# Kernel optimization log

Measured on AMD Instinct MI355X. Metric: run time of the kernel, lower is better.

The kernel has to match this reference:

```python
import jax, jax.numpy as jnp
import numpy as np

N_LAYERS = 200
KSIZE = 7
L_IN = 1388
FC_IN = 188   # 1388 - 200*6
FC_OUT = 91


def setup_inputs() -> dict:
    key = jax.random.key(0)
    k_x, k_w, k_b, k_fw, k_fb = jax.random.split(key, 5)
    B = 1024
    x = jax.random.normal(k_x, (B, L_IN), dtype=jnp.float32)
    # Conv1d(1,1,7) weights: torch default init U(-s, s) with s = 1/sqrt(in_ch*k) = 1/sqrt(7)
    s = 1.0 / np.sqrt(KSIZE)
    conv_w = jax.random.uniform(k_w, (N_LAYERS, KSIZE), dtype=jnp.float32, minval=-s, maxval=s)
    conv_b = jax.random.uniform(k_b, (N_LAYERS,), dtype=jnp.float32, minval=-s, maxval=s)
    sf = 1.0 / np.sqrt(FC_IN)
    fc_w = jax.random.uniform(k_fw, (FC_OUT, FC_IN), dtype=jnp.float32, minval=-sf, maxval=sf)
    fc_b = jax.random.uniform(k_fb, (FC_OUT,), dtype=jnp.float32, minval=-sf, maxval=sf)
    return {"x": x, "conv_w": conv_w, "conv_b": conv_b, "fc_w": fc_w, "fc_b": fc_b}


def _conv1(h, w, b):
    # h: [B, L]; cross-correlation with taps w[0..6], valid padding -> [B, L-6]
    L_out = h.shape[1] - (KSIZE - 1)
    acc = w[0] * h[:, 0:L_out]
    for k in range(1, KSIZE):
        acc = acc + w[k] * h[:, k:k + L_out]
    return acc + b


def reference(x, conv_w, conv_b, fc_w, fc_b):
    h = x  # unsqueeze(1) is implicit: single channel handled as [B, L]
    for i in range(N_LAYERS):
        h = _conv1(h, conv_w[i], conv_b[i])
        if i < N_LAYERS - 1:  # last ReLU was popped in the torch module
            h = jax.nn.relu(h)
    # Linear(188, 91) applied to the length dim, then Sigmoid; squeeze channel dim
    out = jax.nn.sigmoid(h @ fc_w.T + fc_b)  # [B, 91]
    return out
```

## Files before the change

kernel.cpp:

```cpp
#include <hip/hip_runtime.h>
#include <math.h>

#define N_LAYERS 200
#define KSIZE 7
#define L_IN 1388
#define FC_IN 188
#define FC_OUT 91
#define NT 256
#define NW 4
#define NSTAGES 13
#define NGROUPS 50
#define LBUF_N 1352

constexpr int lin_(int s)  { return L_IN - 96 * s; }
constexpr int lout_(int s) { return (s < 12) ? L_IN - 96 * (s + 1) : FC_IN; }
constexpr int nlay_(int s) { return (s < 12) ? 16 : 8; }
constexpr int s_R(int s) {
    const int span = lout_(s) / 4 + 1 + 6 * nlay_(s);
    return (span + 63) / 64;
}

__device__ __forceinline__ float dpp_next(float v) {
    return __int_as_float(
        __builtin_amdgcn_mov_dpp(__float_as_int(v), 0x130, 0xf, 0xf, true));
}

struct __align__(16) WG { float w[32]; };

__device__ __forceinline__ void load_wg(WG& wg, const float4* kb4, int g) {
#pragma unroll
    for (int q = 0; q < 8; ++q)
        *reinterpret_cast<float4*>(&wg.w[4 * q]) = kb4[g * 8 + q];
}

template<int R, bool NR3>
__device__ __forceinline__ void run4(float (&r)[7], const WG& wg) {
#pragma unroll
    for (int jj = 0; jj < 4; ++jj) {
        float h[6];
        {
            constexpr int H1 = (R < 6) ? R : 6;
#pragma unroll
            for (int t = 0; t < H1; ++t) h[t] = dpp_next(r[t]);
#pragma unroll
            for (int t = H1; t < 6; ++t) h[t] = dpp_next(h[t - R]);
        }
        const bool relu = !(NR3 && jj == 3);
#pragma unroll
        for (int j = 0; j < R; ++j) {
            float acc = wg.w[28 + jj];
#pragma unroll
            for (int d = 0; d < KSIZE; ++d) {
                const int m = j + d;
                const float src = (m < R) ? r[m] : h[m - R];
                acc = fmaf(wg.w[jj * 7 + d], src, acc);
            }
            r[j] = relu ? fmaxf(acc, 0.0f) : acc;
        }
    }
}

template<int R, bool FINAL>
__device__ __forceinline__ void run_stage_g(float (&r)[7], WG& A,
        const float4* kb4, int g0, int g1) {
#pragma unroll 1
    for (int g = g0; g < g1; g += 2) {
        WG B;
        load_wg(B, kb4, (g + 1 < NGROUPS) ? g + 1 : NGROUPS - 1);
        run4<R, false>(r, A);
        load_wg(A, kb4, (g + 2 < NGROUPS) ? g + 2 : NGROUPS - 1);
        run4<R, FINAL>(r, B);
    }
}

template<int Ro, int Rn>
__device__ __forceinline__ void repack(float (&r)[7], float* lbuf,
                                       int lane, int co, int co1, int cn) {
#pragma unroll
    for (int j = 0; j < Ro; ++j) {
        const int p = co + lane * Ro + j;
        if (p < co1) lbuf[p] = r[j];
    }
    __syncthreads();
#pragma unroll
    for (int j = 0; j < Rn; ++j) r[j] = lbuf[cn + lane * Rn + j];
    __syncthreads();
}

template<int S>
struct Chain {
    __device__ static __forceinline__ void run(float (&r)[7], WG& A,
        const float4* kb4, float* lbuf, int lane, int wid)
    {
        run_stage_g<s_R(S), false>(r, A, kb4, 4 * S, 4 * S + 4);
        const int co  = (wid * lout_(S)) >> 2;
        const int co1 = ((wid + 1) * lout_(S)) >> 2;
        const int cn  = (wid * lout_(S + 1)) >> 2;
        repack<s_R(S), s_R(S + 1)>(r, lbuf, lane, co, co1, cn);
        Chain<S + 1>::run(r, A, kb4, lbuf, lane, wid);
    }
};

template<>
struct Chain<NSTAGES - 1> {
    __device__ static __forceinline__ void run(float (&r)[7], WG& A,
        const float4* kb4, float* lbuf, int lane, int wid)
    {
        constexpr int R = s_R(NSTAGES - 1);
        run_stage_g<R, true>(r, A, kb4, 48, 50);
        const int co  = (wid * FC_IN) >> 2;
        const int co1 = ((wid + 1) * FC_IN) >> 2;
#pragma unroll
        for (int j = 0; j < R; ++j) {
            const int p = co + lane * R + j;
            if (p < co1) lbuf[p] = r[j];
        }
        __syncthreads();
    }
};

__global__ __launch_bounds__(NT, 4) void conv_chain_kernel(
    const float* __restrict__ x,
    const float* __restrict__ conv_w,
    const float* __restrict__ conv_b,
    const float* __restrict__ fc_w,
    const float* __restrict__ fc_b,
    float* __restrict__ out)
{
    __shared__ __align__(16) float lbuf[LBUF_N];
    __shared__ __align__(16) float kbuf[NGROUPS * 32];

    const int row  = blockIdx.x;
    const int tid  = threadIdx.x;
    const int lane = tid & 63;
    const int wid  = tid >> 6;

    for (int i = tid; i < NGROUPS * 32; i += NT) {
        const int g = i >> 5, t = i & 31;
        kbuf[i] = (t < 28) ? conv_w[g * 28 + t] : conv_b[g * 4 + (t - 28)];
    }
    for (int i = tid; i < LBUF_N; i += NT) lbuf[i] = 0.0f;

    float r[7];
    const float* xr = x + (size_t)row * L_IN;
    const int c0 = (wid * lout_(0)) >> 2;
#pragma unroll
    for (int j = 0; j < 7; ++j) {
        const int p = c0 + lane * 7 + j;
        r[j] = (p < L_IN) ? xr[p] : 0.0f;
    }
    __syncthreads();

    WG A;
    const float4* kb4 = reinterpret_cast<const float4*>(kbuf);
    load_wg(A, kb4, 0);

    Chain<0>::run(r, A, kb4, lbuf, lane, wid);

    if (tid < FC_OUT) {
        float acc = fc_b[tid];
        const float4* wp = (const float4*)(fc_w + tid * FC_IN);
        const float4* hp = (const float4*)lbuf;
#pragma unroll 4
        for (int q = 0; q < FC_IN / 4; ++q) {
            const float4 hv = hp[q];
            const float4 wv = wp[q];
            acc = fmaf(wv.x, hv.x, acc);
            acc = fmaf(wv.y, hv.y, acc);
            acc = fmaf(wv.z, hv.z, acc);
            acc = fmaf(wv.w, hv.w, acc);
        }
        out[(size_t)row * FC_OUT + tid] = 1.0f / (1.0f + expf(-acc));
    }
}

extern "C" void kernel_launch(void* const* d_in, const int* in_sizes, int n_in,
                              void* d_out, int out_size, void* d_ws, size_t ws_size,
                              hipStream_t stream) {
    const float* x      = (const float*)d_in[0];
    const float* conv_w = (const float*)d_in[1];
    const float* conv_b = (const float*)d_in[2];
    const float* fc_w   = (const float*)d_in[3];
    const float* fc_b   = (const float*)d_in[4];
    float* outp = (float*)d_out;

    const int batch = in_sizes[0] / L_IN;
    conv_chain_kernel<<<batch, NT, 0, stream>>>(x, conv_w, conv_b, fc_w, fc_b, outp);
}
```

Baseline: 132.6 us.

## Split each row across two waves and process two rows per block

```diff
diff --git a/kernel.cpp b/kernel.cpp
--- a/kernel.cpp
+++ b/kernel.cpp
@@ -7,17 +7,22 @@
 #define FC_IN 188
 #define FC_OUT 91
 #define NT 256
-#define NW 4
 #define NSTAGES 13
 #define NGROUPS 50
-#define LBUF_N 1352
-
-constexpr int lin_(int s)  { return L_IN - 96 * s; }
-constexpr int lout_(int s) { return (s < 12) ? L_IN - 96 * (s + 1) : FC_IN; }
-constexpr int nlay_(int s) { return (s < 12) ? 16 : 8; }
+#define LBUF_N 1376
+#define RMAX 12
+
+constexpr int s_lo(int s)  { return 16 * s; }
+constexpr int s_hi(int s)  { return (s < 12) ? 16 * s + 16 : N_LAYERS; }
+constexpr int lin_(int s)  { return L_IN - 6 * s_lo(s); }
+constexpr int lout_(int s) { return L_IN - 6 * s_hi(s); }
+constexpr int cut_(int s)  { return lout_(s) / 2; }
+constexpr int marg_(int s) { return 6 * (s_hi(s) - s_lo(s)); }
 constexpr int s_R(int s) {
-    const int span = lout_(s) / 4 + 1 + 6 * nlay_(s);
-    return (span + 63) / 64;
+    const int a = cut_(s) + marg_(s);
+    const int b = lin_(s) - cut_(s);
+    const int m = (a > b) ? a : b;
+    return (m + 63) / 64;
 }
 
 __device__ __forceinline__ float dpp_next(float v) {
@@ -34,7 +39,7 @@
 }
 
 template<int R, bool NR3>
-__device__ __forceinline__ void run4(float (&r)[7], const WG& wg) {
+__device__ __forceinline__ void run4(float (&r)[RMAX], const WG& wg) {
 #pragma unroll
     for (int jj = 0; jj < 4; ++jj) {
         float h[6];
@@ -61,7 +66,7 @@
 }
 
 template<int R, bool FINAL>
-__device__ __forceinline__ void run_stage_g(float (&r)[7], WG& A,
+__device__ __forceinline__ void run_stage_g(float (&r)[RMAX], WG& A,
         const float4* kb4, int g0, int g1) {
 #pragma unroll 1
     for (int g = g0; g < g1; g += 2) {
@@ -74,52 +79,54 @@
 }
 
 template<int Ro, int Rn>
-__device__ __forceinline__ void repack(float (&r)[7], float* lbuf,
-                                       int lane, int co, int co1, int cn) {
+__device__ __forceinline__ void repack(float (&r)[RMAX], float* lbuf,
+                                       int lane, int rwid,
+                                       int cut_o, int lout_o, int cut_n) {
+    const int base  = rwid ? cut_o : 0;
+    const int bound = rwid ? lout_o : cut_o;
 #pragma unroll
     for (int j = 0; j < Ro; ++j) {
-        const int p = co + lane * Ro + j;
-        if (p < co1) lbuf[p] = r[j];
+        const int p = base + lane * Ro + j;
+        if (p < bound) lbuf[p] = r[j];
     }
     __syncthreads();
-#pragma unroll
-    for (int j = 0; j < Rn; ++j) r[j] = lbuf[cn + lane * Rn + j];
+    const int nb = rwid ? cut_n : 0;
+#pragma unroll
+    for (int j = 0; j < Rn; ++j) r[j] = lbuf[nb + lane * Rn + j];
     __syncthreads();
 }
 
 template<int S>
 struct Chain {
-    __device__ static __forceinline__ void run(float (&r)[7], WG& A,
-        const float4* kb4, float* lbuf, int lane, int wid)
+    __device__ static __forceinline__ void run(float (&r)[RMAX], WG& A,
+        const float4* kb4, float* lbuf, int lane, int rwid)
     {
         run_stage_g<s_R(S), false>(r, A, kb4, 4 * S, 4 * S + 4);
-        const int co  = (wid * lout_(S)) >> 2;
-        const int co1 = ((wid + 1) * lout_(S)) >> 2;
-        const int cn  = (wid * lout_(S + 1)) >> 2;
-        repack<s_R(S), s_R(S + 1)>(r, lbuf, lane, co, co1, cn);
-        Chain<S + 1>::run(r, A, kb4, lbuf, lane, wid);
+        repack<s_R(S), s_R(S + 1)>(r, lbuf, lane, rwid,
+                                   cut_(S), lout_(S), cut_(S + 1));
+        Chain<S + 1>::run(r, A, kb4, lbuf, lane, rwid);
     }
 };
 
 template<>
 struct Chain<NSTAGES - 1> {
-    __device__ static __forceinline__ void run(float (&r)[7], WG& A,
-        const float4* kb4, float* lbuf, int lane, int wid)
+    __device__ static __forceinline__ void run(float (&r)[RMAX], WG& A,
+        const float4* kb4, float* lbuf, int lane, int rwid)
     {
         constexpr int R = s_R(NSTAGES - 1);
         run_stage_g<R, true>(r, A, kb4, 48, 50);
-        const int co  = (wid * FC_IN) >> 2;
-        const int co1 = ((wid + 1) * FC_IN) >> 2;
+        const int base  = rwid ? 94 : 0;
+        const int bound = rwid ? 188 : 94;
 #pragma unroll
         for (int j = 0; j < R; ++j) {
-            const int p = co + lane * R + j;
-            if (p < co1) lbuf[p] = r[j];
+            const int p = base + lane * R + j;
+            if (p < bound) lbuf[p] = r[j];
         }
         __syncthreads();
     }
 };
 
-__global__ __launch_bounds__(NT, 4) void conv_chain_kernel(
+__global__ __launch_bounds__(NT, 2) void conv_chain_kernel(
     const float* __restrict__ x,
     const float* __restrict__ conv_w,
     const float* __restrict__ conv_b,
@@ -127,26 +134,31 @@
     const float* __restrict__ fc_b,
     float* __restrict__ out)
 {
-    __shared__ __align__(16) float lbuf[LBUF_N];
+    __shared__ __align__(16) float lbuf[2][LBUF_N];
     __shared__ __align__(16) float kbuf[NGROUPS * 32];
 
-    const int row  = blockIdx.x;
     const int tid  = threadIdx.x;
     const int lane = tid & 63;
     const int wid  = tid >> 6;
+    const int rsel = wid >> 1;
+    const int rwid = wid & 1;
+    const int row  = blockIdx.x * 2 + rsel;
+
+    float* lbufr = lbuf[rsel];
 
     for (int i = tid; i < NGROUPS * 32; i += NT) {
         const int g = i >> 5, t = i & 31;
         kbuf[i] = (t < 28) ? conv_w[g * 28 + t] : conv_b[g * 4 + (t - 28)];
     }
-    for (int i = tid; i < LBUF_N; i += NT) lbuf[i] = 0.0f;
-
-    float r[7];
+    for (int i = tid; i < 2 * LBUF_N; i += NT)
+        lbuf[0][i] = 0.0f;
+
+    float r[RMAX];
     const float* xr = x + (size_t)row * L_IN;
-    const int c0 = (wid * lout_(0)) >> 2;
-#pragma unroll
-    for (int j = 0; j < 7; ++j) {
-        const int p = c0 + lane * 7 + j;
+    const int c0 = rwid ? cut_(0) : 0;
+#pragma unroll
+    for (int j = 0; j < RMAX; ++j) {
+        const int p = c0 + lane * RMAX + j;
         r[j] = (p < L_IN) ? xr[p] : 0.0f;
     }
     __syncthreads();
@@ -155,12 +167,13 @@
     const float4* kb4 = reinterpret_cast<const float4*>(kbuf);
     load_wg(A, kb4, 0);
 
-    Chain<0>::run(r, A, kb4, lbuf, lane, wid);
-
-    if (tid < FC_OUT) {
-        float acc = fc_b[tid];
-        const float4* wp = (const float4*)(fc_w + tid * FC_IN);
-        const float4* hp = (const float4*)lbuf;
+    Chain<0>::run(r, A, kb4, lbufr, lane, rwid);
+
+    const int pt = tid & 127;
+    if (pt < FC_OUT) {
+        float acc = fc_b[pt];
+        const float4* wp = (const float4*)(fc_w + pt * FC_IN);
+        const float4* hp = (const float4*)lbufr;
 #pragma unroll 4
         for (int q = 0; q < FC_IN / 4; ++q) {
             const float4 hv = hp[q];
@@ -170,7 +183,7 @@
             acc = fmaf(wv.z, hv.z, acc);
             acc = fmaf(wv.w, hv.w, acc);
         }
-        out[(size_t)row * FC_OUT + tid] = 1.0f / (1.0f + expf(-acc));
+        out[(size_t)row * FC_OUT + pt] = 1.0f / (1.0f + expf(-acc));
     }
 }
 
@@ -185,5 +198,5 @@
     float* outp = (float*)d_out;
 
     const int batch = in_sizes[0] / L_IN;
-    conv_chain_kernel<<<batch, NT, 0, stream>>>(x, conv_w, conv_b, fc_w, fc_b, outp);
-}
+    conv_chain_kernel<<<batch / 2, NT, 0, stream>>>(x, conv_w, conv_b, fc_w, fc_b, outp);
+}
```

Measured after the change: 120.1 us. -9.5%, faster.
